# Performance work log

Hardware: AMD Instinct MI355X
Metric: run time of the kernel (lower is better)

## Reference

```python
import jax, jax.numpy as jnp
import numpy as np

V, H, L, B = 50257, 1024, 10, 256

def setup_inputs() -> dict:
    key = jax.random.key(0)
    ks = jax.random.split(key, 16)
    s = 0.02
    return {
        "tokens": jax.random.randint(ks[0], (1, B), 0, V),
        "hidden": jax.random.normal(ks[1], (1, B, H), jnp.float32),
        "encoder_outputs": jax.random.normal(ks[2], (L, H), jnp.float32),
        "emb": jax.random.normal(ks[3], (V, H), jnp.float32) * s,
        "attn_W": jax.random.normal(ks[4], (L, 2 * H), jnp.float32) * s,
        "attn_b": jnp.zeros((L,), jnp.float32),
        "comb_W": jax.random.normal(ks[5], (H, 2 * H), jnp.float32) * s,
        "comb_b": jnp.zeros((H,), jnp.float32),
        "W_ih": jax.random.normal(ks[6], (3 * H, H), jnp.float32) * s,
        "W_hh": jax.random.normal(ks[7], (3 * H, H), jnp.float32) * s,
        "b_ih": jnp.zeros((3 * H,), jnp.float32),
        "b_hh": jnp.zeros((3 * H,), jnp.float32),
        "out_W": jax.random.normal(ks[8], (V, H), jnp.float32) * s,
        "out_b": jnp.zeros((V,), jnp.float32),
    }

def reference(tokens, hidden, encoder_outputs, emb, attn_W, attn_b, comb_W, comb_b,
              W_ih, W_hh, b_ih, b_hh, out_W, out_b):
    # Embedding lookup (dropout = identity, eval mode)
    embedded = emb[tokens[0]]            # [B, H]
    h = hidden[-1]                       # [B, H]
    # Attention over encoder outputs
    attn_logits = jnp.concatenate([embedded, h], axis=1) @ attn_W.T + attn_b
    attn_weights = jax.nn.softmax(attn_logits, axis=1)          # [B, L]
    attn_applied = attn_weights @ encoder_outputs                # [B, H]
    # Combine + relu -> GRU input
    x = jnp.concatenate([embedded, attn_applied], axis=1) @ comb_W.T + comb_b
    x = jax.nn.relu(x)                   # [B, H]
    # Single GRU step (PyTorch gate ordering: r, z, n)
    gi = x @ W_ih.T + b_ih               # [B, 3H]
    gh = h @ W_hh.T + b_hh               # [B, 3H]
    i_r, i_z, i_n = jnp.split(gi, 3, axis=1)
    h_r, h_z, h_n = jnp.split(gh, 3, axis=1)
    r = jax.nn.sigmoid(i_r + h_r)
    z = jax.nn.sigmoid(i_z + h_z)
    n = jnp.tanh(i_n + r * h_n)
    h_new = (1.0 - z) * n + z * h        # [B, H]
    # Output projection + log_softmax
    output = jax.nn.log_softmax(h_new @ out_W.T + out_b, axis=1)  # [B, V]
    return (output, h_new[None], attn_weights)
```

## Files before the change

### kernel.cpp

```cpp
#include <hip/hip_runtime.h>
#include <hip/hip_bf16.h>
#include <math.h>
#include <stdint.h>

#define B_SZ 256
#define H_SZ 1024
#define L_SZ 10
#define V_SZ 50257

typedef __attribute__((ext_vector_type(8))) short short8;
typedef __attribute__((ext_vector_type(4))) float floatx4;

__device__ __forceinline__ unsigned f2bf_bits(float f) {
    unsigned u = __float_as_uint(f);
    return (u + 0x7FFFu + ((u >> 16) & 1u)) >> 16;
}

__device__ __forceinline__ short8 cvt8(float4 a, float4 b) {
    short8 r;
    r[0] = (short)f2bf_bits(a.x); r[1] = (short)f2bf_bits(a.y);
    r[2] = (short)f2bf_bits(a.z); r[3] = (short)f2bf_bits(a.w);
    r[4] = (short)f2bf_bits(b.x); r[5] = (short)f2bf_bits(b.y);
    r[6] = (short)f2bf_bits(b.z); r[7] = (short)f2bf_bits(b.w);
    return r;
}

#define WSTRIDE 40

template<int MSUB, int RELU>
__global__ __launch_bounds__(256) void gemm_mfma(
    const float* __restrict__ A, const float* __restrict__ W,
    const float* __restrict__ bias, float* __restrict__ C,
    int N, int K)
{
    __shared__ __align__(16) short lwb[64 * WSTRIDE];

    const int tid  = threadIdx.x;
    const int wave = tid >> 6;
    const int lane = tid & 63;
    const int quad = lane >> 4;
    const int l16  = lane & 15;

    const int n0 = blockIdx.x * 64;
    const int m_base = blockIdx.y * (MSUB * 64) + wave * (MSUB * 16);

    const int wr = tid >> 2;
    const int wc = (tid & 3) * 8;
    const bool wvalid = (n0 + wr) < N;
    const float* wp = W + (size_t)(n0 + wr) * K + wc;

    float4 w0 = make_float4(0.f, 0.f, 0.f, 0.f), w1 = w0;
    if (wvalid) { w0 = *(const float4*)wp; w1 = *(const float4*)(wp + 4); }

    const float* arow[MSUB];
#pragma unroll
    for (int ms = 0; ms < MSUB; ++ms)
        arow[ms] = A + (size_t)(m_base + ms * 16 + l16) * K + quad * 8;

    floatx4 zero = {0.f, 0.f, 0.f, 0.f};
    floatx4 acc[MSUB][4];
#pragma unroll
    for (int ms = 0; ms < MSUB; ++ms)
#pragma unroll
        for (int ns = 0; ns < 4; ++ns) acc[ms][ns] = zero;

    for (int k0 = 0; k0 < K; k0 += 32) {
        __syncthreads();
        *(short8*)&lwb[wr * WSTRIDE + wc] = cvt8(w0, w1);
        __syncthreads();
        if (k0 + 32 < K && wvalid) {
            w0 = *(const float4*)(wp + k0 + 32);
            w1 = *(const float4*)(wp + k0 + 36);
        }
        short8 bfrag[4];
#pragma unroll
        for (int ns = 0; ns < 4; ++ns)
            bfrag[ns] = *(const short8*)&lwb[(ns * 16 + l16) * WSTRIDE + quad * 8];
#pragma unroll
        for (int ms = 0; ms < MSUB; ++ms) {
            float4 a0 = *(const float4*)(arow[ms] + k0);
            float4 a1 = *(const float4*)(arow[ms] + k0 + 4);
            short8 afrag = cvt8(a0, a1);
#pragma unroll
            for (int ns = 0; ns < 4; ++ns)
                acc[ms][ns] = __builtin_amdgcn_mfma_f32_16x16x32_bf16(
                    afrag, bfrag[ns], acc[ms][ns], 0, 0, 0);
        }
    }

    float bia[4];
#pragma unroll
    for (int ns = 0; ns < 4; ++ns) {
        int n = n0 + ns * 16 + l16;
        bia[ns] = (n < N) ? bias[n] : 0.f;
    }
#pragma unroll
    for (int ms = 0; ms < MSUB; ++ms) {
        int mb = m_base + ms * 16 + quad * 4;
#pragma unroll
        for (int ns = 0; ns < 4; ++ns) {
            int n = n0 + ns * 16 + l16;
            if (n < N) {
#pragma unroll
                for (int i = 0; i < 4; ++i) {
                    float v = acc[ms][ns][i] + bia[ns];
                    if (RELU) v = fmaxf(v, 0.f);
                    C[(size_t)(mb + i) * N + n] = v;
                }
            }
        }
    }
}

__global__ __launch_bounds__(256) void attn_kernel(
    const int* __restrict__ tokens, const float* __restrict__ hidden,
    const float* __restrict__ enc, const float* __restrict__ emb,
    const float* __restrict__ attn_W, const float* __restrict__ attn_b,
    float* __restrict__ cat_out, float* __restrict__ attn_w_out)
{
    const int b = blockIdx.x;
    const int tid = threadIdx.x;
    const int tok = tokens[b];
    const float* erow = emb + (size_t)tok * H_SZ;
    const float* hrow = hidden + (size_t)b * H_SZ;

    __shared__ float red[L_SZ][256];
    __shared__ float wts[L_SZ];

    float acc[L_SZ];
#pragma unroll
    for (int l = 0; l < L_SZ; ++l) acc[l] = 0.f;

    for (int i = tid; i < H_SZ; i += 256) {
        float e = erow[i];
        float hv = hrow[i];
        cat_out[(size_t)b * 2 * H_SZ + i] = e;
#pragma unroll
        for (int l = 0; l < L_SZ; ++l) {
            acc[l] += e * attn_W[l * 2 * H_SZ + i] + hv * attn_W[l * 2 * H_SZ + H_SZ + i];
        }
    }
#pragma unroll
    for (int l = 0; l < L_SZ; ++l) red[l][tid] = acc[l];
    __syncthreads();
    for (int s = 128; s > 0; s >>= 1) {
        if (tid < s) {
#pragma unroll
            for (int l = 0; l < L_SZ; ++l) red[l][tid] += red[l][tid + s];
        }
        __syncthreads();
    }
    if (tid == 0) {
        float m = -INFINITY;
        float lg[L_SZ];
#pragma unroll
        for (int l = 0; l < L_SZ; ++l) {
            lg[l] = red[l][0] + attn_b[l];
            m = fmaxf(m, lg[l]);
        }
        float s = 0.f;
#pragma unroll
        for (int l = 0; l < L_SZ; ++l) {
            float e = expf(lg[l] - m);
            wts[l] = e;
            s += e;
        }
        float inv = 1.f / s;
#pragma unroll
        for (int l = 0; l < L_SZ; ++l) {
            wts[l] *= inv;
            attn_w_out[(size_t)b * L_SZ + l] = wts[l];
        }
    }
    __syncthreads();

    for (int i = tid; i < H_SZ; i += 256) {
        float s = 0.f;
#pragma unroll
        for (int l = 0; l < L_SZ; ++l) s += wts[l] * enc[l * H_SZ + i];
        cat_out[(size_t)b * 2 * H_SZ + H_SZ + i] = s;
    }
}

__global__ __launch_bounds__(256) void gru_combine(
    const float* __restrict__ gi, const float* __restrict__ gh,
    const float* __restrict__ hidden, float* __restrict__ h_new)
{
    int idx = blockIdx.x * blockDim.x + threadIdx.x;
    if (idx >= B_SZ * H_SZ) return;
    int b = idx >> 10;
    int j = idx & (H_SZ - 1);
    const float* gib = gi + (size_t)b * 3 * H_SZ;
    const float* ghb = gh + (size_t)b * 3 * H_SZ;
    float i_r = gib[j], i_z = gib[H_SZ + j], i_n = gib[2 * H_SZ + j];
    float h_r = ghb[j], h_z = ghb[H_SZ + j], h_n = ghb[2 * H_SZ + j];
    float r = 1.f / (1.f + expf(-(i_r + h_r)));
    float z = 1.f / (1.f + expf(-(i_z + h_z)));
    float n = tanhf(i_n + r * h_n);
    float h = hidden[idx];
    h_new[idx] = (1.f - z) * n + z * h;
}

__global__ __launch_bounds__(1024) void logsoftmax_v2(float* __restrict__ out)
{
    const int b = blockIdx.x;
    float* row = out + (size_t)b * V_SZ;
    const int tid = threadIdx.x;
    const int wave = tid >> 6;
    const int lane = tid & 63;

    const int head = (int)(((16u - ((uintptr_t)row & 15u)) & 15u) >> 2);
    const int nv = (V_SZ - head) >> 2;
    const float4* r4 = (const float4*)(row + head);
    const int tail_start = head + (nv << 2);

    float m = -INFINITY, s = 0.f;
    if (tid < head) {
        float v = row[tid];
        m = v; s = 1.f;
    }
    for (int i = tid; i < nv; i += 1024) {
        float4 v = r4[i];
        float mv = fmaxf(fmaxf(v.x, v.y), fmaxf(v.z, v.w));
        if (mv > m) { s *= expf(m - mv); m = mv; }
        s += expf(v.x - m) + expf(v.y - m) + expf(v.z - m) + expf(v.w - m);
    }
    for (int i = tail_start + tid; i < V_SZ; i += 1024) {
        float v = row[i];
        if (v > m) { s *= expf(m - v); m = v; }
        s += expf(v - m);
    }

    for (int off = 32; off > 0; off >>= 1) {
        float m2 = __shfl_down(m, off);
        float s2 = __shfl_down(s, off);
        float mn = fmaxf(m, m2);
        s = s * expf(m - mn) + s2 * expf(m2 - mn);
        m = mn;
    }
    __shared__ float smax[16], ssum[16], slse;
    if (lane == 0) { smax[wave] = m; ssum[wave] = s; }
    __syncthreads();
    if (tid == 0) {
        float M = smax[0], S = ssum[0];
        for (int w = 1; w < 16; ++w) {
            float mn = fmaxf(M, smax[w]);
            S = S * expf(M - mn) + ssum[w] * expf(smax[w] - mn);
            M = mn;
        }
        slse = M + logf(S);
    }
    __syncthreads();
    const float lse = slse;

    if (tid < head) row[tid] -= lse;
    float4* w4 = (float4*)(row + head);
    for (int i = tid; i < nv; i += 1024) {
        float4 v = r4[i];
        v.x -= lse; v.y -= lse; v.z -= lse; v.w -= lse;
        w4[i] = v;
    }
    for (int i = tail_start + tid; i < V_SZ; i += 1024) row[i] -= lse;
}

extern "C" void kernel_launch(void* const* d_in, const int* in_sizes, int n_in,
                              void* d_out, int out_size, void* d_ws, size_t ws_size,
                              hipStream_t stream)
{
    const int*   tokens = (const int*)d_in[0];
    const float* hidden = (const float*)d_in[1];
    const float* enc    = (const float*)d_in[2];
    const float* emb    = (const float*)d_in[3];
    const float* attn_W = (const float*)d_in[4];
    const float* attn_b = (const float*)d_in[5];
    const float* comb_W = (const float*)d_in[6];
    const float* comb_b = (const float*)d_in[7];
    const float* W_ih   = (const float*)d_in[8];
    const float* W_hh   = (const float*)d_in[9];
    const float* b_ih   = (const float*)d_in[10];
    const float* b_hh   = (const float*)d_in[11];
    const float* out_W  = (const float*)d_in[12];
    const float* out_b  = (const float*)d_in[13];

    float* out = (float*)d_out;
    float* logits     = out;
    float* h_new      = out + (size_t)B_SZ * V_SZ;
    float* attn_w_out = h_new + (size_t)B_SZ * H_SZ;

    float* cat = logits;
    float* x   = cat + (size_t)B_SZ * 2 * H_SZ;
    float* gi  = x   + (size_t)B_SZ * H_SZ;
    float* gh  = gi  + (size_t)B_SZ * 3 * H_SZ;

    attn_kernel<<<B_SZ, 256, 0, stream>>>(tokens, hidden, enc, emb, attn_W, attn_b,
                                          cat, attn_w_out);
    gemm_mfma<1, 1><<<dim3(H_SZ / 64, 4), 256, 0, stream>>>(
        cat, comb_W, comb_b, x, H_SZ, 2 * H_SZ);
    gemm_mfma<1, 0><<<dim3(3 * H_SZ / 64, 4), 256, 0, stream>>>(
        x, W_ih, b_ih, gi, 3 * H_SZ, H_SZ);
    gemm_mfma<1, 0><<<dim3(3 * H_SZ / 64, 4), 256, 0, stream>>>(
        hidden, W_hh, b_hh, gh, 3 * H_SZ, H_SZ);
    gru_combine<<<(B_SZ * H_SZ + 255) / 256, 256, 0, stream>>>(gi, gh, hidden, h_new);
    gemm_mfma<4, 0><<<dim3((V_SZ + 63) / 64, 1), 256, 0, stream>>>(
        h_new, out_W, out_b, logits, V_SZ, H_SZ);
    logsoftmax_v2<<<B_SZ, 1024, 0, stream>>>(logits);
}
```

Measured before the change: 708.7 us.

## Restructure GEMMs: stage activations in LDS for vocab GEMM, merge GRU gate GEMMs

The vocab projection GEMM now stages the full 256-row activation tile in LDS as bf16, and each wave streams its own 16 output columns of weights directly from global memory, giving 16 MFMAs per weight fragment. The small GEMMs drop LDS and use 16-column tiles with per-wave 64-row blocks, and the W_ih and W_hh GEMMs are merged into one launch via blockIdx.y. The float-to-bf16 conversion switches to a cheaper perm-based round-half-up pack. This aims to cut the overhead of repeated weight conversion and LDS traffic and to remove one launch, at the cost of slightly different rounding and less weight reuse in the small GEMMs.

Result: slower. 763.1 us (+7.7%).

```diff
diff --git a/kernel.cpp b/kernel.cpp
--- a/kernel.cpp
+++ b/kernel.cpp
@@ -11,103 +11,139 @@
 typedef __attribute__((ext_vector_type(8))) short short8;
 typedef __attribute__((ext_vector_type(4))) float floatx4;
 
-__device__ __forceinline__ unsigned f2bf_bits(float f) {
-    unsigned u = __float_as_uint(f);
-    return (u + 0x7FFFu + ((u >> 16) & 1u)) >> 16;
-}
-
-__device__ __forceinline__ short8 cvt8(float4 a, float4 b) {
-    short8 r;
-    r[0] = (short)f2bf_bits(a.x); r[1] = (short)f2bf_bits(a.y);
-    r[2] = (short)f2bf_bits(a.z); r[3] = (short)f2bf_bits(a.w);
-    r[4] = (short)f2bf_bits(b.x); r[5] = (short)f2bf_bits(b.y);
-    r[6] = (short)f2bf_bits(b.z); r[7] = (short)f2bf_bits(b.w);
-    return r;
-}
-
-#define WSTRIDE 40
-
-template<int MSUB, int RELU>
-__global__ __launch_bounds__(256) void gemm_mfma(
+__device__ __forceinline__ unsigned pack2(float lo, float hi) {
+    unsigned a = __float_as_uint(hi) + 0x8000u;
+    unsigned b = __float_as_uint(lo) + 0x8000u;
+    return __builtin_amdgcn_perm(a, b, 0x07060302u);
+}
+__device__ __forceinline__ short8 pack8(float4 a, float4 b) {
+    union { unsigned u[4]; short8 s; } r;
+    r.u[0] = pack2(a.x, a.y); r.u[1] = pack2(a.z, a.w);
+    r.u[2] = pack2(b.x, b.y); r.u[3] = pack2(b.z, b.w);
+    return r.s;
+}
+
+#define ASTRIDE 40
+
+__global__ __launch_bounds__(256) void gemm_big(
     const float* __restrict__ A, const float* __restrict__ W,
-    const float* __restrict__ bias, float* __restrict__ C,
-    int N, int K)
-{
-    __shared__ __align__(16) short lwb[64 * WSTRIDE];
+    const float* __restrict__ bias, float* __restrict__ C, int N, int K)
+{
+    __shared__ __align__(16) short alds[256 * ASTRIDE];
 
     const int tid  = threadIdx.x;
-    const int wave = tid >> 6;
-    const int lane = tid & 63;
-    const int quad = lane >> 4;
-    const int l16  = lane & 15;
-
-    const int n0 = blockIdx.x * 64;
-    const int m_base = blockIdx.y * (MSUB * 64) + wave * (MSUB * 16);
-
-    const int wr = tid >> 2;
-    const int wc = (tid & 3) * 8;
-    const bool wvalid = (n0 + wr) < N;
-    const float* wp = W + (size_t)(n0 + wr) * K + wc;
-
-    float4 w0 = make_float4(0.f, 0.f, 0.f, 0.f), w1 = w0;
-    if (wvalid) { w0 = *(const float4*)wp; w1 = *(const float4*)(wp + 4); }
-
-    const float* arow[MSUB];
-#pragma unroll
-    for (int ms = 0; ms < MSUB; ++ms)
-        arow[ms] = A + (size_t)(m_base + ms * 16 + l16) * K + quad * 8;
-
-    floatx4 zero = {0.f, 0.f, 0.f, 0.f};
-    floatx4 acc[MSUB][4];
-#pragma unroll
-    for (int ms = 0; ms < MSUB; ++ms)
-#pragma unroll
-        for (int ns = 0; ns < 4; ++ns) acc[ms][ns] = zero;
+    const int wave = tid >> 6, lane = tid & 63;
+    const int quad = lane >> 4, l16 = lane & 15;
+
+    const int n0 = blockIdx.x * 64 + wave * 16;
+    int wrow = n0 + l16; if (wrow > N - 1) wrow = N - 1;
+    const float* wp = W + (size_t)wrow * K + quad * 8;
+    const float* ap = A + (size_t)tid * K;
+
+    float4 wr0 = *(const float4*)(wp);
+    float4 wr1 = *(const float4*)(wp + 4);
+    float4 ar[8];
+#pragma unroll
+    for (int j = 0; j < 8; ++j) ar[j] = *(const float4*)(ap + 4 * j);
+
+    floatx4 acc[16];
+#pragma unroll
+    for (int ms = 0; ms < 16; ++ms) acc[ms] = (floatx4){0.f, 0.f, 0.f, 0.f};
+
+    short* arow = alds + tid * ASTRIDE;
 
     for (int k0 = 0; k0 < K; k0 += 32) {
         __syncthreads();
-        *(short8*)&lwb[wr * WSTRIDE + wc] = cvt8(w0, w1);
+#pragma unroll
+        for (int j = 0; j < 4; ++j) {
+            union { unsigned u[4]; int4 v; } d;
+            d.u[0] = pack2(ar[2*j].x,   ar[2*j].y);
+            d.u[1] = pack2(ar[2*j].z,   ar[2*j].w);
+            d.u[2] = pack2(ar[2*j+1].x, ar[2*j+1].y);
+            d.u[3] = pack2(ar[2*j+1].z, ar[2*j+1].w);
+            *(int4*)(arow + j * 8) = d.v;
+        }
         __syncthreads();
-        if (k0 + 32 < K && wvalid) {
-            w0 = *(const float4*)(wp + k0 + 32);
-            w1 = *(const float4*)(wp + k0 + 36);
-        }
-        short8 bfrag[4];
-#pragma unroll
-        for (int ns = 0; ns < 4; ++ns)
-            bfrag[ns] = *(const short8*)&lwb[(ns * 16 + l16) * WSTRIDE + quad * 8];
-#pragma unroll
-        for (int ms = 0; ms < MSUB; ++ms) {
-            float4 a0 = *(const float4*)(arow[ms] + k0);
-            float4 a1 = *(const float4*)(arow[ms] + k0 + 4);
-            short8 afrag = cvt8(a0, a1);
-#pragma unroll
-            for (int ns = 0; ns < 4; ++ns)
-                acc[ms][ns] = __builtin_amdgcn_mfma_f32_16x16x32_bf16(
-                    afrag, bfrag[ns], acc[ms][ns], 0, 0, 0);
-        }
-    }
-
-    float bia[4];
-#pragma unroll
-    for (int ns = 0; ns < 4; ++ns) {
-        int n = n0 + ns * 16 + l16;
-        bia[ns] = (n < N) ? bias[n] : 0.f;
-    }
-#pragma unroll
-    for (int ms = 0; ms < MSUB; ++ms) {
-        int mb = m_base + ms * 16 + quad * 4;
-#pragma unroll
-        for (int ns = 0; ns < 4; ++ns) {
-            int n = n0 + ns * 16 + l16;
-            if (n < N) {
-#pragma unroll
-                for (int i = 0; i < 4; ++i) {
-                    float v = acc[ms][ns][i] + bia[ns];
-                    if (RELU) v = fmaxf(v, 0.f);
-                    C[(size_t)(mb + i) * N + n] = v;
-                }
-            }
+
+        short8 bfrag = pack8(wr0, wr1);
+
+        if (k0 + 32 < K) {
+            wr0 = *(const float4*)(wp + k0 + 32);
+            wr1 = *(const float4*)(wp + k0 + 36);
+#pragma unroll
+            for (int j = 0; j < 8; ++j)
+                ar[j] = *(const float4*)(ap + k0 + 32 + 4 * j);
+        }
+
+#pragma unroll
+        for (int ms = 0; ms < 16; ++ms) {
+            short8 afrag = *(const short8*)(alds + (ms * 16 + l16) * ASTRIDE + quad * 8);
+            acc[ms] = __builtin_amdgcn_mfma_f32_16x16x32_bf16(afrag, bfrag, acc[ms], 0, 0, 0);
+        }
+    }
+
+    const int coln = n0 + l16;
+    if (coln < N) {
+        const float bv = bias[coln];
+#pragma unroll
+        for (int ms = 0; ms < 16; ++ms) {
+            const int rbase = ms * 16 + quad * 4;
+#pragma unroll
+            for (int i = 0; i < 4; ++i)
+                C[(size_t)(rbase + i) * N + coln] = acc[ms][i] + bv;
+        }
+    }
+}
+
+template<int RELU>
+__global__ __launch_bounds__(256) void gemm_small(
+    const float* __restrict__ A,  const float* __restrict__ W,
+    const float* __restrict__ bias,  float* __restrict__ C,
+    const float* __restrict__ A2, const float* __restrict__ W2,
+    const float* __restrict__ bias2, float* __restrict__ C2,
+    int N, int K)
+{
+    if (blockIdx.y == 1) { A = A2; W = W2; bias = bias2; C = C2; }
+
+    const int tid  = threadIdx.x;
+    const int wave = tid >> 6, lane = tid & 63;
+    const int quad = lane >> 4, l16 = lane & 15;
+
+    const int n0 = blockIdx.x * 16;
+    const int m0 = wave * 64;
+
+    const float* wp  = W + (size_t)(n0 + l16) * K + quad * 8;
+    const float* ap0 = A + (size_t)(m0 + l16) * K + quad * 8;
+
+    floatx4 acc[4];
+#pragma unroll
+    for (int ms = 0; ms < 4; ++ms) acc[ms] = (floatx4){0.f, 0.f, 0.f, 0.f};
+
+#pragma unroll 2
+    for (int k0 = 0; k0 < K; k0 += 32) {
+        float4 w0 = *(const float4*)(wp + k0);
+        float4 w1 = *(const float4*)(wp + k0 + 4);
+        short8 bfrag = pack8(w0, w1);
+#pragma unroll
+        for (int ms = 0; ms < 4; ++ms) {
+            const float* a = ap0 + (size_t)(ms * 16) * K + k0;
+            float4 a0 = *(const float4*)(a);
+            float4 a1 = *(const float4*)(a + 4);
+            short8 afrag = pack8(a0, a1);
+            acc[ms] = __builtin_amdgcn_mfma_f32_16x16x32_bf16(afrag, bfrag, acc[ms], 0, 0, 0);
+        }
+    }
+
+    const int coln = n0 + l16;
+    const float bv = bias[coln];
+#pragma unroll
+    for (int ms = 0; ms < 4; ++ms) {
+        const int rbase = m0 + ms * 16 + quad * 4;
+#pragma unroll
+        for (int i = 0; i < 4; ++i) {
+            float v = acc[ms][i] + bv;
+            if (RELU) v = fmaxf(v, 0.f);
+            C[(size_t)(rbase + i) * N + coln] = v;
         }
     }
 }
@@ -215,10 +251,7 @@
     const int tail_start = head + (nv << 2);
 
     float m = -INFINITY, s = 0.f;
-    if (tid < head) {
-        float v = row[tid];
-        m = v; s = 1.f;
-    }
+    if (tid < head) { float v = row[tid]; m = v; s = 1.f; }
     for (int i = tid; i < nv; i += 1024) {
         float4 v = r4[i];
         float mv = fmaxf(fmaxf(v.x, v.y), fmaxf(v.z, v.w));
@@ -294,14 +327,12 @@
 
     attn_kernel<<<B_SZ, 256, 0, stream>>>(tokens, hidden, enc, emb, attn_W, attn_b,
                                           cat, attn_w_out);
-    gemm_mfma<1, 1><<<dim3(H_SZ / 64, 4), 256, 0, stream>>>(
-        cat, comb_W, comb_b, x, H_SZ, 2 * H_SZ);
-    gemm_mfma<1, 0><<<dim3(3 * H_SZ / 64, 4), 256, 0, stream>>>(
-        x, W_ih, b_ih, gi, 3 * H_SZ, H_SZ);
-    gemm_mfma<1, 0><<<dim3(3 * H_SZ / 64, 4), 256, 0, stream>>>(
-        hidden, W_hh, b_hh, gh, 3 * H_SZ, H_SZ);
+    gemm_small<1><<<dim3(H_SZ / 16, 1), 256, 0, stream>>>(
+        cat, comb_W, comb_b, x,  cat, comb_W, comb_b, x,  H_SZ, 2 * H_SZ);
+    gemm_small<0><<<dim3(3 * H_SZ / 16, 2), 256, 0, stream>>>(
+        x, W_ih, b_ih, gi,  hidden, W_hh, b_hh, gh,  3 * H_SZ, H_SZ);
     gru_combine<<<(B_SZ * H_SZ + 255) / 256, 256, 0, stream>>>(gi, gh, hidden, h_new);
-    gemm_mfma<4, 0><<<dim3((V_SZ + 63) / 64, 1), 256, 0, stream>>>(
+    gemm_big<<<dim3((V_SZ + 63) / 64, 1), 256, 0, stream>>>(
         h_new, out_W, out_b, logits, V_SZ, H_SZ);
     logsoftmax_v2<<<B_SZ, 1024, 0, stream>>>(logits);
 }
```
